# Kernel optimization log

Measured on AMD Instinct MI355X. Metric: run time of the kernel, lower is better.

Reference implementation:

```python
import jax, jax.numpy as jnp
import numpy as np

E = 800_000      # number of edges
DIN = 128        # in_channels
DMID = 256       # mid_channels
DOUT = 128       # output_channels
V = 50_000       # number of vertices (segments)


def setup_inputs() -> dict:
    key = jax.random.key(0)
    k1, k2, k3, k4, k5 = jax.random.split(key, 5)
    x = jax.random.normal(k1, (E, DIN), dtype=jnp.float32)
    vertex_id = jax.random.randint(k2, (E,), 0, V)
    W1 = jax.random.normal(k3, (DIN, DMID), dtype=jnp.float32) * (1.0 / np.sqrt(DIN))
    b1 = jax.random.normal(k4, (DMID,), dtype=jnp.float32) * 0.01
    W2 = jax.random.normal(k5, (DIN + DMID, DOUT), dtype=jnp.float32) * (1.0 / np.sqrt(DIN + DMID))
    return {"x": x, "vertex_id": vertex_id, "W1": W1, "b1": b1, "W2": W2, "num_vertices": V}


def reference(x, vertex_id, W1, b1, W2, num_vertices):
    # first_process: Linear(DIN -> DMID)                        (E, DMID)
    z = x @ W1 + b1
    # aggregator: scatter_max over vertex segments              (V, DMID)
    z_max = jax.ops.segment_max(z, vertex_id, num_segments=num_vertices)
    # formatter: index_select gather back to edges              (E, DMID)
    z_vertex = jnp.take(z_max, vertex_id, axis=0)
    # merger: concat along feature dim                          (E, DIN+DMID)
    z_merged = jnp.concatenate([x, z_vertex], axis=-1)
    # second_process: Linear(DIN+DMID -> DOUT, bias=False)      (E, DOUT)
    return z_merged @ W2
```

## Files before the change

kernel.cpp:

```cpp
#include <hip/hip_runtime.h>

#define DIN   128
#define DMID  256
#define DOUT  128
#define VNUM  50000

typedef __attribute__((ext_vector_type(8))) __bf16 bf16x8;
typedef __attribute__((ext_vector_type(4))) float  f32x4;

static __device__ __forceinline__ unsigned short b16(float f) {
  union { __bf16 b; unsigned short u; } r; r.b = (__bf16)f; return r.u;
}
static __device__ __forceinline__ unsigned pk2(float lo, float hi) {
  union { __bf16 b[2]; unsigned u; } r;
  r.b[0] = (__bf16)lo; r.b[1] = (__bf16)hi;
  return r.u;
}
static __device__ __forceinline__ unsigned unflip_bits(unsigned m) {
  unsigned mask = ((int)m < 0) ? 0x80000000u : 0xFFFFFFFFu;
  return m ^ mask;
}
static __device__ __forceinline__ unsigned flip32_from16(unsigned m) {
  return (m << 16) | ((m & 0x8000u) ? 0u : 0xFFFFu);
}

__global__ void k_hist(const int* __restrict__ vid, int* __restrict__ counts, int E) {
  int i = blockIdx.x * blockDim.x + threadIdx.x;
  if (i < E) atomicAdd(counts + vid[i], 1);
}

__global__ __launch_bounds__(1024) void k_scan(int* __restrict__ cursor, int V) {
  __shared__ int wsum[16];
  const int tid = threadIdx.x, lane = tid & 63, wv = tid >> 6;
  int carry = 0;
  for (int base = 0; base < V; base += 1024) {
    const int idx = base + tid;
    const int c = (idx < V) ? cursor[idx] : 0;
    int s = c;
#pragma unroll
    for (int d = 1; d < 64; d <<= 1) {
      int t = __shfl_up(s, d, 64);
      if (lane >= d) s += t;
    }
    if (lane == 63) wsum[wv] = s;
    __syncthreads();
    if (wv == 0 && lane < 16) {
      int ws = wsum[lane];
#pragma unroll
      for (int d = 1; d < 16; d <<= 1) {
        int t = __shfl_up(ws, d, 16);
        if (lane >= d) ws += t;
      }
      wsum[lane] = ws;
    }
    __syncthreads();
    const int woff = (wv == 0) ? 0 : wsum[wv - 1];
    if (idx < V) cursor[idx] = carry + woff + (s - c);
    carry += wsum[15];
    __syncthreads();
  }
}

__global__ void k_scatter(const int* __restrict__ vid, int* __restrict__ cursor,
                          int* __restrict__ sorted, int E) {
  int i = blockIdx.x * blockDim.x + threadIdx.x;
  if (i < E) {
    int v = vid[i];
    int p = atomicAdd(cursor + v, 1);
    sorted[p] = i;
  }
}

__global__ __launch_bounds__(512) void k_gemm1_max(
    const float* __restrict__ x, const int* __restrict__ vid,
    const int* __restrict__ sorted, const float* __restrict__ W1,
    const float* __restrict__ b1, unsigned* __restrict__ zu, int ntiles) {
  __shared__ unsigned short lx[64 * 136];
  __shared__ unsigned short zt[256 * 70];
  __shared__ int lvid[64];

  const int tid  = threadIdx.x;
  const int lane = tid & 63;
  const int w    = tid >> 6;
  const int l15  = lane & 15;
  const int l4   = lane >> 4;
  const int row8 = tid >> 3;
  const int s8   = tid & 7;

  bf16x8 bfrag[4][2];
  float  bias[2];
#pragma unroll
  for (int ni = 0; ni < 2; ++ni) {
    const int col = w * 32 + ni * 16 + l15;
    bias[ni] = b1[col];
#pragma unroll
    for (int kk = 0; kk < 4; ++kk) {
      union { bf16x8 v; unsigned short u[8]; } tmp;
#pragma unroll
      for (int j = 0; j < 8; ++j)
        tmp.u[j] = b16(W1[(kk * 32 + l4 * 8 + j) * DMID + col]);
      bfrag[kk][ni] = tmp.v;
    }
  }

  for (int t = blockIdx.x; t < ntiles; t += gridDim.x) {
    if (tid < 64) lvid[tid] = vid[sorted[t * 64 + tid]];
    {
      const int eid = sorted[t * 64 + row8];
      const float4* src =
          reinterpret_cast<const float4*>(x + (size_t)eid * DIN + s8 * 16);
#pragma unroll
      for (int i = 0; i < 4; ++i) {
        float4 v = src[i];
        uint2 o = { pk2(v.x, v.y), pk2(v.z, v.w) };
        *reinterpret_cast<uint2*>(&lx[row8 * 136 + s8 * 16 + i * 4]) = o;
      }
    }
    __syncthreads();

    const int myv = lvid[lane];
    const int nv  = (lane == 63) ? (myv ^ 1) : lvid[lane + 1];
    const unsigned long long emask = __ballot(myv != nv);
    const bool contOpen = (lvid[31] == lvid[32]);

    f32x4 acc[4][2];
#pragma unroll
    for (int mi = 0; mi < 4; ++mi)
#pragma unroll
      for (int ni = 0; ni < 2; ++ni)
        acc[mi][ni] = (f32x4){bias[ni], bias[ni], bias[ni], bias[ni]};
#pragma unroll
    for (int kk = 0; kk < 4; ++kk) {
      bf16x8 a[4];
#pragma unroll
      for (int mi = 0; mi < 4; ++mi)
        a[mi] = *reinterpret_cast<const bf16x8*>(
            &lx[(mi * 16 + l15) * 136 + kk * 32 + l4 * 8]);
#pragma unroll
      for (int mi = 0; mi < 4; ++mi)
#pragma unroll
        for (int ni = 0; ni < 2; ++ni)
          acc[mi][ni] = __builtin_amdgcn_mfma_f32_16x16x32_bf16(
              a[mi], bfrag[kk][ni], acc[mi][ni], 0, 0, 0);
    }

    {
      unsigned* ztw = reinterpret_cast<unsigned*>(zt);
#pragma unroll
      for (int ni = 0; ni < 2; ++ni) {
        const int col = w * 32 + ni * 16 + l15;
        const int cb  = col * 35 + l4 * 2;
#pragma unroll
        for (int mi = 0; mi < 4; ++mi)
#pragma unroll
          for (int p = 0; p < 2; ++p) {
            unsigned tpk = pk2(acc[mi][ni][2 * p], acc[mi][ni][2 * p + 1]);
            unsigned mflip = 0x80008000u + ((tpk >> 15) & 0x00010001u) * 0x7FFFu;
            ztw[cb + mi * 8 + p] = tpk ^ mflip;
          }
      }
    }
    __syncthreads();

    {
      const int col = tid & 255;
      const int h   = tid >> 8;
      const unsigned* zc = reinterpret_cast<const unsigned*>(&zt[col * 70 + h * 32]);
      unsigned cur = 0;
      bool first = true;
#pragma unroll
      for (int p = 0; p < 16; ++p) {
        const unsigned pr = zc[p];
#pragma unroll
        for (int j = 0; j < 2; ++j) {
          const unsigned val = j ? (pr >> 16) : (pr & 0xFFFFu);
          cur = val > cur ? val : cur;
          const int row = h * 32 + p * 2 + j;
          if ((emask >> row) & 1) {
            const int v = lvid[row];
            const unsigned enc = flip32_from16(cur);
            unsigned* ad = zu + (size_t)v * DMID + col;
            if (row == 63 || (first && (h == 0 || contOpen))) atomicMax(ad, enc);
            else *ad = enc;
            cur = 0; first = false;
          }
        }
      }
      if (h == 0 && !((emask >> 31) & 1)) {
        const int v = lvid[31];
        atomicMax(zu + (size_t)v * DMID + col, flip32_from16(cur));
      }
    }
    __syncthreads();
  }
}

__global__ __launch_bounds__(256) void k_ymm(
    const unsigned* __restrict__ zu, const float* __restrict__ W2,
    float* __restrict__ Y, int ntiles) {
  extern __shared__ unsigned short sm[];
  unsigned short* w2bt = sm;
  unsigned short* za   = sm + 128 * 264;

  const int tid  = threadIdx.x;
  const int lane = tid & 63;
  const int w    = tid >> 6;
  const int wr   = w >> 1, wc = w & 1;
  const int l15  = lane & 15, l4 = lane >> 4;

  {
    const int n = tid & 127, kh = tid >> 7;
    for (int k = kh * 128; k < kh * 128 + 128; ++k)
      w2bt[n * 264 + k] = b16(W2[(size_t)(DIN + k) * DOUT + n]);
  }
  __syncthreads();

  for (int t = blockIdx.x; t < ntiles; t += gridDim.x) {
    {
      const int row = tid >> 2, q = tid & 3;
      const int v = t * 64 + row;
      unsigned short* dz = &za[row * 264 + q * 64];
      if (v < VNUM) {
        const uint4* sz = reinterpret_cast<const uint4*>(zu + (size_t)v * DMID + q * 64);
#pragma unroll
        for (int i = 0; i < 16; ++i) {
          uint4 m = sz[i];
          ushort4 o = { (unsigned short)(unflip_bits(m.x) >> 16),
                        (unsigned short)(unflip_bits(m.y) >> 16),
                        (unsigned short)(unflip_bits(m.z) >> 16),
                        (unsigned short)(unflip_bits(m.w) >> 16) };
          *reinterpret_cast<ushort4*>(dz + i * 4) = o;
        }
      } else {
        ushort4 zo = {0, 0, 0, 0};
#pragma unroll
        for (int i = 0; i < 16; ++i) *reinterpret_cast<ushort4*>(dz + i * 4) = zo;
      }
    }
    __syncthreads();

    f32x4 acc[2][4];
#pragma unroll
    for (int mi = 0; mi < 2; ++mi)
#pragma unroll
      for (int ni = 0; ni < 4; ++ni) acc[mi][ni] = (f32x4){0.f, 0.f, 0.f, 0.f};

#pragma unroll
    for (int kk = 0; kk < 8; ++kk) {
      bf16x8 a[2], b[4];
#pragma unroll
      for (int mi = 0; mi < 2; ++mi)
        a[mi] = *reinterpret_cast<const bf16x8*>(
            &za[(wr * 32 + mi * 16 + l15) * 264 + kk * 32 + l4 * 8]);
#pragma unroll
      for (int ni = 0; ni < 4; ++ni)
        b[ni] = *reinterpret_cast<const bf16x8*>(
            &w2bt[(wc * 64 + ni * 16 + l15) * 264 + kk * 32 + l4 * 8]);
#pragma unroll
      for (int mi = 0; mi < 2; ++mi)
#pragma unroll
        for (int ni = 0; ni < 4; ++ni)
          acc[mi][ni] = __builtin_amdgcn_mfma_f32_16x16x32_bf16(
              a[mi], b[ni], acc[mi][ni], 0, 0, 0);
    }

#pragma unroll
    for (int mi = 0; mi < 2; ++mi)
#pragma unroll
      for (int r = 0; r < 4; ++r) {
        const int v = t * 64 + wr * 32 + mi * 16 + l4 * 4 + r;
        if (v < VNUM) {
          float* o = Y + (size_t)v * DOUT + wc * 64 + l15;
#pragma unroll
          for (int ni = 0; ni < 4; ++ni) o[ni * 16] = acc[mi][ni][r];
        }
      }
    __syncthreads();
  }
}

__global__ __launch_bounds__(256, 3) void k_gemm2(
    const float* __restrict__ x, const int* __restrict__ vid,
    const float* __restrict__ W2, const float* __restrict__ Y,
    float* __restrict__ out, int ntiles) {
  __shared__ unsigned short w2at[128 * 136];
  __shared__ unsigned short lx[64 * 136];
  __shared__ int lvid[64];

  const int tid  = threadIdx.x;
  const int lane = tid & 63;
  const int w    = tid >> 6;
  const int wr   = w >> 1, wc = w & 1;
  const int l15  = lane & 15, l4 = lane >> 4;

  {
    const int n = tid & 127, kh = tid >> 7;
    for (int k = kh * 64; k < kh * 64 + 64; ++k)
      w2at[n * 136 + k] = b16(W2[(size_t)k * DOUT + n]);
  }
  __syncthreads();

  for (int t = blockIdx.x; t < ntiles; t += gridDim.x) {
    {
      const int row = tid >> 2, q = tid & 3;
      const float4* sx =
          reinterpret_cast<const float4*>(x + (size_t)(t * 64 + row) * DIN + q * 32);
#pragma unroll
      for (int i = 0; i < 8; ++i) {
        float4 v = sx[i];
        uint2 o = { pk2(v.x, v.y), pk2(v.z, v.w) };
        *reinterpret_cast<uint2*>(&lx[row * 136 + q * 32 + i * 4]) = o;
      }
      if (tid < 64) lvid[tid] = vid[t * 64 + tid];
    }
    __syncthreads();

    f32x4 acc[2][4];
#pragma unroll
    for (int mi = 0; mi < 2; ++mi)
#pragma unroll
      for (int ni = 0; ni < 4; ++ni) acc[mi][ni] = (f32x4){0.f, 0.f, 0.f, 0.f};

#pragma unroll
    for (int kk = 0; kk < 4; ++kk) {
      bf16x8 a[2], b[4];
#pragma unroll
      for (int mi = 0; mi < 2; ++mi)
        a[mi] = *reinterpret_cast<const bf16x8*>(
            &lx[(wr * 32 + mi * 16 + l15) * 136 + kk * 32 + l4 * 8]);
#pragma unroll
      for (int ni = 0; ni < 4; ++ni)
        b[ni] = *reinterpret_cast<const bf16x8*>(
            &w2at[(wc * 64 + ni * 16 + l15) * 136 + kk * 32 + l4 * 8]);
#pragma unroll
      for (int mi = 0; mi < 2; ++mi)
#pragma unroll
        for (int ni = 0; ni < 4; ++ni)
          acc[mi][ni] = __builtin_amdgcn_mfma_f32_16x16x32_bf16(
              a[mi], b[ni], acc[mi][ni], 0, 0, 0);
    }

#pragma unroll
    for (int mi = 0; mi < 2; ++mi)
#pragma unroll
      for (int r = 0; r < 4; ++r) {
        const int row = wr * 32 + mi * 16 + l4 * 4 + r;
        const float* Yr = Y + (size_t)lvid[row] * DOUT + wc * 64 + l15;
        float* o = out + (size_t)(t * 64 + row) * DOUT + wc * 64 + l15;
#pragma unroll
        for (int ni = 0; ni < 4; ++ni) o[ni * 16] = acc[mi][ni][r] + Yr[ni * 16];
      }
    __syncthreads();
  }
}

extern "C" void kernel_launch(void* const* d_in, const int* in_sizes, int n_in,
                              void* d_out, int out_size, void* d_ws, size_t ws_size,
                              hipStream_t stream) {
  const float* x   = (const float*)d_in[0];
  const int*   vid = (const int*)d_in[1];
  const float* W1  = (const float*)d_in[2];
  const float* b1  = (const float*)d_in[3];
  const float* W2  = (const float*)d_in[4];
  float* out = (float*)d_out;

  const int E = in_sizes[1];
  const int ntiles = E / 64;
  const int ntY = (VNUM + 63) / 64;

  char* ws = (char*)d_ws;
  unsigned* zu = (unsigned*)ws;
  int* cnt     = (int*)(ws + (size_t)VNUM * DMID * 4);
  int* sorted  = (int*)(ws + (size_t)VNUM * DMID * 4 + VNUM * 4);
  float* Y     = (float*)(ws + (size_t)VNUM * DMID * 4 + VNUM * 4 + (size_t)E * 4);

  hipMemsetAsync(zu, 0, (size_t)VNUM * DMID * 4 + VNUM * 4, stream);

  k_hist<<<(E + 255) / 256, 256, 0, stream>>>(vid, cnt, E);
  k_scan<<<1, 1024, 0, stream>>>(cnt, VNUM);
  k_scatter<<<(E + 255) / 256, 256, 0, stream>>>(vid, cnt, sorted, E);

  k_gemm1_max<<<2048, 512, 0, stream>>>(x, vid, sorted, W1, b1, zu, ntiles);

  const int smY = (128 * 264 + 64 * 264) * sizeof(unsigned short);
  hipFuncSetAttribute((const void*)k_ymm,
                      hipFuncAttributeMaxDynamicSharedMemorySize, smY);
  k_ymm<<<782, 256, smY, stream>>>(zu, W2, Y, ntY);

  k_gemm2<<<768, 256, 0, stream>>>(x, vid, W2, Y, out, ntiles);
}
```

Baseline: 668.6 us.

## Parallelize vertex-count scan and prefetch next gathered x tile in gemm1

The single-block serial prefix scan over vertex counts is replaced by a three-kernel reduce/top-scan/fix scan spread across many blocks, which removes a long single-workgroup latency step. In the gemm1+segment-max kernel, the gathered x rows and vertex ids for the next tile are loaded into registers while the current tile's max-reduction and atomics run, then written to LDS afterwards, using a double-buffered lvid array. This aims to hide gather latency behind the scatter phase, at the cost of extra register pressure and two more kernel launches.

```diff
diff --git a/kernel.cpp b/kernel.cpp
--- a/kernel.cpp
+++ b/kernel.cpp
@@ -29,36 +29,52 @@
   if (i < E) atomicAdd(counts + vid[i], 1);
 }
 
-__global__ __launch_bounds__(1024) void k_scan(int* __restrict__ cursor, int V) {
-  __shared__ int wsum[16];
+__global__ __launch_bounds__(256) void k_scan_red(
+    const int* __restrict__ cnt, int* __restrict__ bsum, int V) {
+  __shared__ int ws[4];
+  const int i = blockIdx.x * 256 + threadIdx.x;
+  int c = (i < V) ? cnt[i] : 0;
+#pragma unroll
+  for (int d = 1; d < 64; d <<= 1) c += __shfl_xor(c, d);
+  if ((threadIdx.x & 63) == 0) ws[threadIdx.x >> 6] = c;
+  __syncthreads();
+  if (threadIdx.x == 0) bsum[blockIdx.x] = ws[0] + ws[1] + ws[2] + ws[3];
+}
+
+__global__ __launch_bounds__(256) void k_scan_top(int* __restrict__ bsum, int nb) {
+  __shared__ int ws[4];
   const int tid = threadIdx.x, lane = tid & 63, wv = tid >> 6;
-  int carry = 0;
-  for (int base = 0; base < V; base += 1024) {
-    const int idx = base + tid;
-    const int c = (idx < V) ? cursor[idx] : 0;
-    int s = c;
-#pragma unroll
-    for (int d = 1; d < 64; d <<= 1) {
-      int t = __shfl_up(s, d, 64);
-      if (lane >= d) s += t;
-    }
-    if (lane == 63) wsum[wv] = s;
-    __syncthreads();
-    if (wv == 0 && lane < 16) {
-      int ws = wsum[lane];
-#pragma unroll
-      for (int d = 1; d < 16; d <<= 1) {
-        int t = __shfl_up(ws, d, 16);
-        if (lane >= d) ws += t;
-      }
-      wsum[lane] = ws;
-    }
-    __syncthreads();
-    const int woff = (wv == 0) ? 0 : wsum[wv - 1];
-    if (idx < V) cursor[idx] = carry + woff + (s - c);
-    carry += wsum[15];
-    __syncthreads();
-  }
+  int c = (tid < nb) ? bsum[tid] : 0;
+  int s = c;
+#pragma unroll
+  for (int d = 1; d < 64; d <<= 1) {
+    int u = __shfl_up(s, d, 64);
+    if (lane >= d) s += u;
+  }
+  if (lane == 63) ws[wv] = s;
+  __syncthreads();
+  int off = 0;
+  for (int k = 0; k < wv; ++k) off += ws[k];
+  if (tid < nb) bsum[tid] = off + (s - c);
+}
+
+__global__ __launch_bounds__(256) void k_scan_fix(
+    int* __restrict__ cursor, const int* __restrict__ bsum, int V) {
+  __shared__ int ws[4];
+  const int i = blockIdx.x * 256 + threadIdx.x;
+  const int lane = threadIdx.x & 63, wv = threadIdx.x >> 6;
+  int c = (i < V) ? cursor[i] : 0;
+  int s = c;
+#pragma unroll
+  for (int d = 1; d < 64; d <<= 1) {
+    int u = __shfl_up(s, d, 64);
+    if (lane >= d) s += u;
+  }
+  if (lane == 63) ws[wv] = s;
+  __syncthreads();
+  int off = bsum[blockIdx.x];
+  for (int k = 0; k < wv; ++k) off += ws[k];
+  if (i < V) cursor[i] = off + (s - c);
 }
 
 __global__ void k_scatter(const int* __restrict__ vid, int* __restrict__ cursor,
@@ -77,7 +93,7 @@
     const float* __restrict__ b1, unsigned* __restrict__ zu, int ntiles) {
   __shared__ unsigned short lx[64 * 136];
   __shared__ unsigned short zt[256 * 70];
-  __shared__ int lvid[64];
+  __shared__ int lvid[2][64];
 
   const int tid  = threadIdx.x;
   const int lane = tid & 63;
@@ -86,6 +102,7 @@
   const int l4   = lane >> 4;
   const int row8 = tid >> 3;
   const int s8   = tid & 7;
+  const int G    = gridDim.x;
 
   bf16x8 bfrag[4][2];
   float  bias[2];
@@ -103,25 +120,37 @@
     }
   }
 
-  for (int t = blockIdx.x; t < ntiles; t += gridDim.x) {
-    if (tid < 64) lvid[tid] = vid[sorted[t * 64 + tid]];
-    {
-      const int eid = sorted[t * 64 + row8];
-      const float4* src =
-          reinterpret_cast<const float4*>(x + (size_t)eid * DIN + s8 * 16);
-#pragma unroll
-      for (int i = 0; i < 4; ++i) {
-        float4 v = src[i];
-        uint2 o = { pk2(v.x, v.y), pk2(v.z, v.w) };
-        *reinterpret_cast<uint2*>(&lx[row8 * 136 + s8 * 16 + i * 4]) = o;
-      }
-    }
-    __syncthreads();
-
-    const int myv = lvid[lane];
-    const int nv  = (lane == 63) ? (myv ^ 1) : lvid[lane + 1];
+  const int t0 = blockIdx.x;
+  if (t0 >= ntiles) return;
+
+  {
+    if (tid < 64) lvid[0][tid] = vid[sorted[t0 * 64 + tid]];
+    const int eid = sorted[t0 * 64 + row8];
+    const float4* src =
+        reinterpret_cast<const float4*>(x + (size_t)eid * DIN + s8 * 16);
+#pragma unroll
+    for (int i = 0; i < 4; ++i) {
+      float4 v = src[i];
+      uint2 o = { pk2(v.x, v.y), pk2(v.z, v.w) };
+      *reinterpret_cast<uint2*>(&lx[row8 * 136 + s8 * 16 + i * 4]) = o;
+    }
+  }
+  __syncthreads();
+
+  int cur = 0;
+  for (int t = t0; t < ntiles; t += G, cur ^= 1) {
+    const int tn = t + G;
+    const bool more = (tn < ntiles);
+    int eidN = 0, sidN = 0;
+    if (more) {
+      eidN = sorted[tn * 64 + row8];
+      if (tid < 64) sidN = sorted[tn * 64 + tid];
+    }
+
+    const int myv = lvid[cur][lane];
+    const int nv  = (lane == 63) ? (myv ^ 1) : lvid[cur][lane + 1];
     const unsigned long long emask = __ballot(myv != nv);
-    const bool contOpen = (lvid[31] == lvid[32]);
+    const bool contOpen = (lvid[cur][31] == lvid[cur][32]);
 
     f32x4 acc[4][2];
 #pragma unroll
@@ -162,11 +191,20 @@
     }
     __syncthreads();
 
+    float4 x0, x1, x2, x3;
+    int vN = 0;
+    if (more) {
+      const float4* src =
+          reinterpret_cast<const float4*>(x + (size_t)eidN * DIN + s8 * 16);
+      x0 = src[0]; x1 = src[1]; x2 = src[2]; x3 = src[3];
+      if (tid < 64) vN = vid[sidN];
+    }
+
     {
       const int col = tid & 255;
       const int h   = tid >> 8;
       const unsigned* zc = reinterpret_cast<const unsigned*>(&zt[col * 70 + h * 32]);
-      unsigned cur = 0;
+      unsigned curm = 0;
       bool first = true;
 #pragma unroll
       for (int p = 0; p < 16; ++p) {
@@ -174,22 +212,35 @@
 #pragma unroll
         for (int j = 0; j < 2; ++j) {
           const unsigned val = j ? (pr >> 16) : (pr & 0xFFFFu);
-          cur = val > cur ? val : cur;
+          curm = val > curm ? val : curm;
           const int row = h * 32 + p * 2 + j;
           if ((emask >> row) & 1) {
-            const int v = lvid[row];
-            const unsigned enc = flip32_from16(cur);
+            const int v = lvid[cur][row];
+            const unsigned enc = flip32_from16(curm);
             unsigned* ad = zu + (size_t)v * DMID + col;
             if (row == 63 || (first && (h == 0 || contOpen))) atomicMax(ad, enc);
             else *ad = enc;
-            cur = 0; first = false;
+            curm = 0; first = false;
           }
         }
       }
       if (h == 0 && !((emask >> 31) & 1)) {
-        const int v = lvid[31];
-        atomicMax(zu + (size_t)v * DMID + col, flip32_from16(cur));
-      }
+        const int v = lvid[cur][31];
+        atomicMax(zu + (size_t)v * DMID + col, flip32_from16(curm));
+      }
+    }
+
+    if (more) {
+      uint2 o0 = { pk2(x0.x, x0.y), pk2(x0.z, x0.w) };
+      uint2 o1 = { pk2(x1.x, x1.y), pk2(x1.z, x1.w) };
+      uint2 o2 = { pk2(x2.x, x2.y), pk2(x2.z, x2.w) };
+      uint2 o3 = { pk2(x3.x, x3.y), pk2(x3.z, x3.w) };
+      unsigned short* dst = &lx[row8 * 136 + s8 * 16];
+      *reinterpret_cast<uint2*>(dst + 0)  = o0;
+      *reinterpret_cast<uint2*>(dst + 4)  = o1;
+      *reinterpret_cast<uint2*>(dst + 8)  = o2;
+      *reinterpret_cast<uint2*>(dst + 12) = o3;
+      if (tid < 64) lvid[cur ^ 1][tid] = vN;
     }
     __syncthreads();
   }
@@ -367,17 +418,22 @@
   const int E = in_sizes[1];
   const int ntiles = E / 64;
   const int ntY = (VNUM + 63) / 64;
+  const int nb = (VNUM + 255) / 256;
 
   char* ws = (char*)d_ws;
-  unsigned* zu = (unsigned*)ws;
-  int* cnt     = (int*)(ws + (size_t)VNUM * DMID * 4);
-  int* sorted  = (int*)(ws + (size_t)VNUM * DMID * 4 + VNUM * 4);
-  float* Y     = (float*)(ws + (size_t)VNUM * DMID * 4 + VNUM * 4 + (size_t)E * 4);
+  size_t off = 0;
+  unsigned* zu = (unsigned*)(ws + off); off += (size_t)VNUM * DMID * 4;
+  int* cnt     = (int*)(ws + off);      off += (size_t)VNUM * 4;
+  int* sorted  = (int*)(ws + off);      off += (size_t)E * 4;
+  float* Y     = (float*)(ws + off);    off += (size_t)VNUM * DOUT * 4;
+  int* bsum    = (int*)(ws + off);      off += 256 * 4;
 
   hipMemsetAsync(zu, 0, (size_t)VNUM * DMID * 4 + VNUM * 4, stream);
 
   k_hist<<<(E + 255) / 256, 256, 0, stream>>>(vid, cnt, E);
-  k_scan<<<1, 1024, 0, stream>>>(cnt, VNUM);
+  k_scan_red<<<nb, 256, 0, stream>>>(cnt, bsum, VNUM);
+  k_scan_top<<<1, 256, 0, stream>>>(bsum, nb);
+  k_scan_fix<<<nb, 256, 0, stream>>>(cnt, bsum, VNUM);
   k_scatter<<<(E + 255) / 256, 256, 0, stream>>>(vid, cnt, sorted, E);
 
   k_gemm1_max<<<2048, 512, 0, stream>>>(x, vid, sorted, W1, b1, zu, ntiles);
```

New measurement: 608.4 us. 9.0% less time.
